# Performance work log

Hardware: AMD Instinct MI355X
Metric: run time of the kernel (lower is better)

The kernel has to match this reference:

```python
import jax, jax.numpy as jnp
import numpy as np

N = 16384      # number of target nodes
NS = 16384     # number of source nodes
K = 32         # neighbors per node
CS = 256       # source_channels
CT = 256       # target_channels
CO = 64        # out_channels
M = 64         # size (number of weight matrices); must equal CO for the original code to broadcast


def setup_inputs() -> dict:
    key = jax.random.key(0)
    ks = jax.random.split(key, 9)
    source = jax.random.normal(ks[0], (NS, CS), dtype=jnp.float32)
    target = jax.random.normal(ks[1], (N, CT), dtype=jnp.float32)
    neighbors = jax.random.randint(ks[2], (N, K), 0, NS)
    # size parallel Linear(CS, CO) layers, stored [in, out]
    W_lin = jax.random.normal(ks[3], (M, CS, CO), dtype=jnp.float32) / np.sqrt(CS)
    b_lin = jax.random.normal(ks[4], (M, CO), dtype=jnp.float32) * 0.01
    # source assignment Linear(CS, M)
    W_s = jax.random.normal(ks[5], (CS, M), dtype=jnp.float32) / np.sqrt(CS)
    b_s = jax.random.normal(ks[6], (M,), dtype=jnp.float32) * 0.01
    # target assignment Linear(CT, M)
    W_t = jax.random.normal(ks[7], (CT, M), dtype=jnp.float32) / np.sqrt(CT)
    b_t = jax.random.normal(ks[8], (M,), dtype=jnp.float32) * 0.01
    return {"source": source, "target": target, "neighbors": neighbors,
            "W_lin": W_lin, "b_lin": b_lin, "W_s": W_s, "b_s": b_s,
            "W_t": W_t, "b_t": b_t}


def reference(source, target, neighbors, W_lin, b_lin, W_s, b_s, W_t, b_t):
    # gather neighbor messages: [N, K, CS]
    msgs = source[neighbors]
    # assignment logits: source proj [N, K, M] + target proj broadcast [N, 1, M]
    s_logit = jnp.einsum('nkc,cm->nkm', msgs, W_s) + b_s
    t_logit = target @ W_t + b_t                      # [N, M]
    assignment = jax.nn.softmax(s_logit + t_logit[:, None, :], axis=-1)  # [N, K, M]
    # (assignment * stack_m(msgs @ W_m)).mean over m == assignment * (msgs @ mean_m W_m)
    # because assignment is independent of m (faithful to the original math).
    W_mean = W_lin.mean(axis=0)                       # [CS, CO]
    b_mean = b_lin.mean(axis=0)                       # [CO]
    proj = jnp.einsum('nkc,co->nko', msgs, W_mean) + b_mean  # [N, K, CO]
    return assignment * proj                          # [N, K, CO]  (CO == M)
```

## Files before the change

kernel.cpp:

```cpp
#include <hip/hip_runtime.h>
#include <hip/hip_fp16.h>

typedef _Float16 f16x8 __attribute__((ext_vector_type(8)));
typedef _Float16 f16x4 __attribute__((ext_vector_type(4)));
typedef float f32x4 __attribute__((ext_vector_type(4)));

__global__ void prep_weights(const float* __restrict__ W_lin, const float* __restrict__ b_lin,
                             const float* __restrict__ W_s, const float* __restrict__ W_t,
                             _Float16* __restrict__ WcT, _Float16* __restrict__ Wt16,
                             float* __restrict__ bmean) {
    int tid = blockIdx.x * 256 + threadIdx.x;
    if (tid < 16384) {
        int c = tid >> 6, o = tid & 63;
        WcT[o * 256 + c]  = (_Float16)W_s[c * 64 + o];
        Wt16[o * 256 + c] = (_Float16)W_t[c * 64 + o];
    } else {
        int t = tid - 16384;
        int c = t >> 6, o = t & 63;
        float s = 0.f;
        #pragma unroll 8
        for (int m = 0; m < 64; ++m) s += W_lin[m * 16384 + c * 64 + o];
        WcT[(64 + o) * 256 + c] = (_Float16)(s * (1.f / 64.f));
    }
    if (tid < 64) {
        float s = 0.f;
        #pragma unroll 8
        for (int m = 0; m < 64; ++m) s += b_lin[m * 64 + tid];
        bmean[tid] = s * (1.f / 64.f);
    }
}

__device__ __forceinline__ f16x8 cvt8(const float* p) {
    f32x4 x = *(const f32x4*)p;
    f32x4 y = *(const f32x4*)(p + 4);
    f16x8 h;
    h[0] = (_Float16)x[0]; h[1] = (_Float16)x[1]; h[2] = (_Float16)x[2]; h[3] = (_Float16)x[3];
    h[4] = (_Float16)y[0]; h[5] = (_Float16)y[1]; h[6] = (_Float16)y[2]; h[7] = (_Float16)y[3];
    return h;
}

__global__ __launch_bounds__(256, 2)
void gemm_prep(const float* __restrict__ source, const float* __restrict__ target,
               const _Float16* __restrict__ WcT, const _Float16* __restrict__ Wt16,
               const float* __restrict__ bmean, const float* __restrict__ b_s,
               const float* __restrict__ b_t,
               _Float16* __restrict__ Pe, _Float16* __restrict__ Pp,
               float* __restrict__ Et) {
    __shared__ _Float16 lds[32768];

    const int tid = threadIdx.x;
    const int w = tid >> 6, l = tid & 63;
    const int l15 = l & 15, lq = l >> 4;
    const int b = blockIdx.x;

    if (b < 256) {
        const int rb = b * 64;
        const float* arow = source + (size_t)(rb + w * 16 + l15) * 256;
        f16x8 af[8];
        #pragma unroll
        for (int s = 0; s < 8; ++s) af[s] = cvt8(arow + s * 32 + lq * 8);

        #pragma unroll
        for (int i = 0; i < 16; ++i) {
            int c = i * 256 + tid;
            int fi = c >> 6, lane = c & 63;
            int nt = fi >> 3, s = fi & 7;
            f16x8 v = *(const f16x8*)(WcT + (nt * 16 + (lane & 15)) * 256 + s * 32 + (lane >> 4) * 8);
            *(f16x8*)((char*)lds + c * 16) = v;
        }
        __syncthreads();

        const char* bb = (const char*)lds + l * 16;
        f32x4 acc[8] = {};
        #pragma unroll
        for (int s = 0; s < 8; ++s) {
            #pragma unroll
            for (int nt = 0; nt < 8; ++nt) {
                f16x8 bf = *(const f16x8*)(bb + nt * 8192 + s * 1024);
                acc[nt] = __builtin_amdgcn_mfma_f32_16x16x32_f16(af[s], bf, acc[nt], 0, 0, 0);
            }
        }

        float bmv[4];
        #pragma unroll
        for (int nt = 0; nt < 4; ++nt) bmv[nt] = bmean[nt * 16 + l15];
        #pragma unroll
        for (int j = 0; j < 4; ++j) {
            int row = rb + w * 16 + lq * 4 + j;
            #pragma unroll
            for (int nt = 0; nt < 4; ++nt) {
                Pe[row * 64 + nt * 16 + l15] = (_Float16)__expf(acc[nt][j]);
                Pp[row * 64 + nt * 16 + l15] = (_Float16)(acc[nt + 4][j] + bmv[nt]);
            }
        }
    } else {
        const int rb = (b - 256) * 64;
        const float* arow = target + (size_t)(rb + w * 16 + l15) * 256;
        f16x8 af[8];
        #pragma unroll
        for (int s = 0; s < 8; ++s) af[s] = cvt8(arow + s * 32 + lq * 8);

        #pragma unroll
        for (int i = 0; i < 8; ++i) {
            int c = i * 256 + tid;
            int fi = c >> 6, lane = c & 63;
            int nt = fi >> 3, s = fi & 7;
            f16x8 v = *(const f16x8*)(Wt16 + (nt * 16 + (lane & 15)) * 256 + s * 32 + (lane >> 4) * 8);
            *(f16x8*)((char*)lds + c * 16) = v;
        }
        __syncthreads();

        const char* bb = (const char*)lds + l * 16;
        f32x4 acc[4] = {};
        #pragma unroll
        for (int s = 0; s < 8; ++s) {
            #pragma unroll
            for (int nt = 0; nt < 4; ++nt) {
                f16x8 bf = *(const f16x8*)(bb + nt * 8192 + s * 1024);
                acc[nt] = __builtin_amdgcn_mfma_f32_16x16x32_f16(af[s], bf, acc[nt], 0, 0, 0);
            }
        }

        float bsv[4];
        #pragma unroll
        for (int nt = 0; nt < 4; ++nt) {
            int col = nt * 16 + l15;
            bsv[nt] = b_s[col] + b_t[col];
        }
        #pragma unroll
        for (int j = 0; j < 4; ++j) {
            int row = rb + w * 16 + lq * 4 + j;
            #pragma unroll
            for (int nt = 0; nt < 4; ++nt)
                Et[row * 64 + nt * 16 + l15] = __expf(acc[nt][j] + bsv[nt]);
        }
    }
}

__global__ __launch_bounds__(256)
void epilogue(const int* __restrict__ neighbors, const _Float16* __restrict__ Pe,
              const _Float16* __restrict__ Pp, const float* __restrict__ Et,
              float* __restrict__ out) {
    const int tid = threadIdx.x;
    const int w = tid >> 6, l = tid & 63;
    const int lq = l >> 4, l15 = l & 15;
    const int n = blockIdx.x * 4 + w;
    const int co = l15 * 4;

    f32x4 et = *(const f32x4*)(Et + n * 64 + co);

    int nb[8];
    #pragma unroll
    for (int g = 0; g < 8; ++g) nb[g] = neighbors[n * 32 + g * 4 + lq];

    f16x4 pe[8], pp[8];
    #pragma unroll
    for (int g = 0; g < 2; ++g) {
        pe[g] = *(const f16x4*)(Pe + nb[g] * 64 + co);
        pp[g] = *(const f16x4*)(Pp + nb[g] * 64 + co);
    }

    #pragma unroll
    for (int g = 0; g < 8; ++g) {
        if (g + 2 < 8) {
            pe[g + 2] = *(const f16x4*)(Pe + nb[g + 2] * 64 + co);
            pp[g + 2] = *(const f16x4*)(Pp + nb[g + 2] * 64 + co);
        }
        float w0 = (float)pe[g][0] * et[0];
        float w1 = (float)pe[g][1] * et[1];
        float w2 = (float)pe[g][2] * et[2];
        float w3 = (float)pe[g][3] * et[3];
        float s = (w0 + w1) + (w2 + w3);
        s += __shfl_xor(s, 1);
        s += __shfl_xor(s, 2);
        s += __shfl_xor(s, 4);
        s += __shfl_xor(s, 8);
        float inv = 1.0f / s;
        f32x4 o;
        o[0] = w0 * inv * (float)pp[g][0];
        o[1] = w1 * inv * (float)pp[g][1];
        o[2] = w2 * inv * (float)pp[g][2];
        o[3] = w3 * inv * (float)pp[g][3];
        *(f32x4*)(out + (size_t)(n * 32 + g * 4 + lq) * 64 + co) = o;
    }
}

extern "C" void kernel_launch(void* const* d_in, const int* in_sizes, int n_in,
                              void* d_out, int out_size, void* d_ws, size_t ws_size,
                              hipStream_t stream) {
    const float* source    = (const float*)d_in[0];
    const float* target    = (const float*)d_in[1];
    const int*   neighbors = (const int*)d_in[2];
    const float* W_lin     = (const float*)d_in[3];
    const float* b_lin     = (const float*)d_in[4];
    const float* W_s       = (const float*)d_in[5];
    const float* b_s       = (const float*)d_in[6];
    const float* W_t       = (const float*)d_in[7];
    const float* b_t       = (const float*)d_in[8];

    char* ws = (char*)d_ws;
    _Float16* Pe    = (_Float16*)ws;
    _Float16* Pp    = (_Float16*)(ws + (2u << 20));
    float*    Et    = (float*)(ws + (4u << 20));
    _Float16* WcT   = (_Float16*)(ws + (8u << 20));
    _Float16* Wt16  = (_Float16*)(ws + (8u << 20) + 65536);
    float*    bmean = (float*)(ws + (8u << 20) + 98304);
    float*    out   = (float*)d_out;

    prep_weights<<<128, 256, 0, stream>>>(W_lin, b_lin, W_s, W_t, WcT, Wt16, bmean);
    gemm_prep<<<512, 256, 0, stream>>>(source, target, WcT, Wt16, bmean, b_s, b_t,
                                       Pe, Pp, Et);
    epilogue<<<4096, 256, 0, stream>>>(neighbors, Pe, Pp, Et, out);
}
```

Before: 55.43 us.

## Interleave Pe/Pp rows, drop LDS staging, split GEMM columns across waves

```diff
diff --git a/kernel.cpp b/kernel.cpp
--- a/kernel.cpp
+++ b/kernel.cpp
@@ -39,108 +39,81 @@
     return h;
 }
 
-__global__ __launch_bounds__(256, 2)
+__global__ __launch_bounds__(256, 4)
 void gemm_prep(const float* __restrict__ source, const float* __restrict__ target,
                const _Float16* __restrict__ WcT, const _Float16* __restrict__ Wt16,
                const float* __restrict__ bmean, const float* __restrict__ b_s,
                const float* __restrict__ b_t,
-               _Float16* __restrict__ Pe, _Float16* __restrict__ Pp,
-               float* __restrict__ Et) {
-    __shared__ _Float16 lds[32768];
-
+               _Float16* __restrict__ Ppe, float* __restrict__ Et) {
     const int tid = threadIdx.x;
     const int w = tid >> 6, l = tid & 63;
     const int l15 = l & 15, lq = l >> 4;
     const int b = blockIdx.x;
 
-    if (b < 256) {
-        const int rb = b * 64;
-        const float* arow = source + (size_t)(rb + w * 16 + l15) * 256;
+    if (b < 1024) {
+        const int rb = b * 16;
+        const float* arow = source + (size_t)(rb + l15) * 256;
         f16x8 af[8];
         #pragma unroll
         for (int s = 0; s < 8; ++s) af[s] = cvt8(arow + s * 32 + lq * 8);
 
-        #pragma unroll
-        for (int i = 0; i < 16; ++i) {
-            int c = i * 256 + tid;
-            int fi = c >> 6, lane = c & 63;
-            int nt = fi >> 3, s = fi & 7;
-            f16x8 v = *(const f16x8*)(WcT + (nt * 16 + (lane & 15)) * 256 + s * 32 + (lane >> 4) * 8);
-            *(f16x8*)((char*)lds + c * 16) = v;
-        }
-        __syncthreads();
+        const int nt0 = w * 2;
+        const _Float16* b0p = WcT + (nt0 * 16 + l15) * 256 + lq * 8;
+        const _Float16* b1p = b0p + 16 * 256;
 
-        const char* bb = (const char*)lds + l * 16;
-        f32x4 acc[8] = {};
+        f32x4 acc[2] = {};
         #pragma unroll
         for (int s = 0; s < 8; ++s) {
-            #pragma unroll
-            for (int nt = 0; nt < 8; ++nt) {
-                f16x8 bf = *(const f16x8*)(bb + nt * 8192 + s * 1024);
-                acc[nt] = __builtin_amdgcn_mfma_f32_16x16x32_f16(af[s], bf, acc[nt], 0, 0, 0);
-            }
+            f16x8 b0 = *(const f16x8*)(b0p + s * 32);
+            f16x8 b1 = *(const f16x8*)(b1p + s * 32);
+            acc[0] = __builtin_amdgcn_mfma_f32_16x16x32_f16(af[s], b0, acc[0], 0, 0, 0);
+            acc[1] = __builtin_amdgcn_mfma_f32_16x16x32_f16(af[s], b1, acc[1], 0, 0, 0);
         }
 
-        float bmv[4];
+        const bool isPe = (nt0 < 4);
+        float addv[2];
         #pragma unroll
-        for (int nt = 0; nt < 4; ++nt) bmv[nt] = bmean[nt * 16 + l15];
+        for (int t = 0; t < 2; ++t)
+            addv[t] = isPe ? 0.f : bmean[(nt0 + t - 4) * 16 + l15];
+
         #pragma unroll
         for (int j = 0; j < 4; ++j) {
-            int row = rb + w * 16 + lq * 4 + j;
+            int row = rb + lq * 4 + j;
             #pragma unroll
-            for (int nt = 0; nt < 4; ++nt) {
-                Pe[row * 64 + nt * 16 + l15] = (_Float16)__expf(acc[nt][j]);
-                Pp[row * 64 + nt * 16 + l15] = (_Float16)(acc[nt + 4][j] + bmv[nt]);
+            for (int t = 0; t < 2; ++t) {
+                float v = acc[t][j];
+                _Float16 r = isPe ? (_Float16)__expf(v) : (_Float16)(v + addv[t]);
+                Ppe[row * 128 + (nt0 + t) * 16 + l15] = r;
             }
         }
     } else {
-        const int rb = (b - 256) * 64;
-        const float* arow = target + (size_t)(rb + w * 16 + l15) * 256;
+        const int rb = (b - 1024) * 16;
+        const float* arow = target + (size_t)(rb + l15) * 256;
         f16x8 af[8];
         #pragma unroll
         for (int s = 0; s < 8; ++s) af[s] = cvt8(arow + s * 32 + lq * 8);
 
-        #pragma unroll
-        for (int i = 0; i < 8; ++i) {
-            int c = i * 256 + tid;
-            int fi = c >> 6, lane = c & 63;
-            int nt = fi >> 3, s = fi & 7;
-            f16x8 v = *(const f16x8*)(Wt16 + (nt * 16 + (lane & 15)) * 256 + s * 32 + (lane >> 4) * 8);
-            *(f16x8*)((char*)lds + c * 16) = v;
-        }
-        __syncthreads();
-
-        const char* bb = (const char*)lds + l * 16;
-        f32x4 acc[4] = {};
+        const _Float16* bp = Wt16 + (w * 16 + l15) * 256 + lq * 8;
+        f32x4 acc = {};
         #pragma unroll
         for (int s = 0; s < 8; ++s) {
-            #pragma unroll
-            for (int nt = 0; nt < 4; ++nt) {
-                f16x8 bf = *(const f16x8*)(bb + nt * 8192 + s * 1024);
-                acc[nt] = __builtin_amdgcn_mfma_f32_16x16x32_f16(af[s], bf, acc[nt], 0, 0, 0);
-            }
+            f16x8 bf = *(const f16x8*)(bp + s * 32);
+            acc = __builtin_amdgcn_mfma_f32_16x16x32_f16(af[s], bf, acc, 0, 0, 0);
         }
 
-        float bsv[4];
-        #pragma unroll
-        for (int nt = 0; nt < 4; ++nt) {
-            int col = nt * 16 + l15;
-            bsv[nt] = b_s[col] + b_t[col];
-        }
+        const int col = w * 16 + l15;
+        const float bsv = b_s[col] + b_t[col];
         #pragma unroll
         for (int j = 0; j < 4; ++j) {
-            int row = rb + w * 16 + lq * 4 + j;
-            #pragma unroll
-            for (int nt = 0; nt < 4; ++nt)
-                Et[row * 64 + nt * 16 + l15] = __expf(acc[nt][j] + bsv[nt]);
+            int row = rb + lq * 4 + j;
+            Et[row * 64 + col] = __expf(acc[j] + bsv);
         }
     }
 }
 
 __global__ __launch_bounds__(256)
-void epilogue(const int* __restrict__ neighbors, const _Float16* __restrict__ Pe,
-              const _Float16* __restrict__ Pp, const float* __restrict__ Et,
-              float* __restrict__ out) {
+void epilogue(const int* __restrict__ neighbors, const _Float16* __restrict__ Ppe,
+              const float* __restrict__ Et, float* __restrict__ out) {
     const int tid = threadIdx.x;
     const int w = tid >> 6, l = tid & 63;
     const int lq = l >> 4, l15 = l & 15;
@@ -156,15 +129,15 @@
     f16x4 pe[8], pp[8];
     #pragma unroll
     for (int g = 0; g < 2; ++g) {
-        pe[g] = *(const f16x4*)(Pe + nb[g] * 64 + co);
-        pp[g] = *(const f16x4*)(Pp + nb[g] * 64 + co);
+        pe[g] = *(const f16x4*)(Ppe + nb[g] * 128 + co);
+        pp[g] = *(const f16x4*)(Ppe + nb[g] * 128 + 64 + co);
     }
 
     #pragma unroll
     for (int g = 0; g < 8; ++g) {
         if (g + 2 < 8) {
-            pe[g + 2] = *(const f16x4*)(Pe + nb[g + 2] * 64 + co);
-            pp[g + 2] = *(const f16x4*)(Pp + nb[g + 2] * 64 + co);
+            pe[g + 2] = *(const f16x4*)(Ppe + nb[g + 2] * 128 + co);
+            pp[g + 2] = *(const f16x4*)(Ppe + nb[g + 2] * 128 + 64 + co);
         }
         float w0 = (float)pe[g][0] * et[0];
         float w1 = (float)pe[g][1] * et[1];
@@ -181,7 +154,7 @@
         o[1] = w1 * inv * (float)pp[g][1];
         o[2] = w2 * inv * (float)pp[g][2];
         o[3] = w3 * inv * (float)pp[g][3];
-        *(f32x4*)(out + (size_t)(n * 32 + g * 4 + lq) * 64 + co) = o;
+        __builtin_nontemporal_store(o, (f32x4*)(out + (size_t)(n * 32 + g * 4 + lq) * 64 + co));
     }
 }
 
@@ -199,8 +172,7 @@
     const float* b_t       = (const float*)d_in[8];
 
     char* ws = (char*)d_ws;
-    _Float16* Pe    = (_Float16*)ws;
-    _Float16* Pp    = (_Float16*)(ws + (2u << 20));
+    _Float16* Ppe   = (_Float16*)ws;
     float*    Et    = (float*)(ws + (4u << 20));
     _Float16* WcT   = (_Float16*)(ws + (8u << 20));
     _Float16* Wt16  = (_Float16*)(ws + (8u << 20) + 65536);
@@ -208,7 +180,7 @@
     float*    out   = (float*)d_out;
 
     prep_weights<<<128, 256, 0, stream>>>(W_lin, b_lin, W_s, W_t, WcT, Wt16, bmean);
-    gemm_prep<<<512, 256, 0, stream>>>(source, target, WcT, Wt16, bmean, b_s, b_t,
-                                       Pe, Pp, Et);
-    epilogue<<<4096, 256, 0, stream>>>(neighbors, Pe, Pp, Et, out);
+    gemm_prep<<<2048, 256, 0, stream>>>(source, target, WcT, Wt16, bmean, b_s, b_t,
+                                        Ppe, Et);
+    epilogue<<<4096, 256, 0, stream>>>(neighbors, Ppe, Et, out);
 }
```

New measurement: 64.78 us. 16.9% more time.

## Interleave Pe/Pp rows and process two nodes per wave with all gathers issued upfront

Applied to the files above, without the earlier changes.

```diff
diff --git a/kernel.cpp b/kernel.cpp
--- a/kernel.cpp
+++ b/kernel.cpp
@@ -44,8 +44,7 @@
                const _Float16* __restrict__ WcT, const _Float16* __restrict__ Wt16,
                const float* __restrict__ bmean, const float* __restrict__ b_s,
                const float* __restrict__ b_t,
-               _Float16* __restrict__ Pe, _Float16* __restrict__ Pp,
-               float* __restrict__ Et) {
+               _Float16* __restrict__ Ppe, float* __restrict__ Et) {
     __shared__ _Float16 lds[32768];
 
     const int tid = threadIdx.x;
@@ -89,8 +88,8 @@
             int row = rb + w * 16 + lq * 4 + j;
             #pragma unroll
             for (int nt = 0; nt < 4; ++nt) {
-                Pe[row * 64 + nt * 16 + l15] = (_Float16)__expf(acc[nt][j]);
-                Pp[row * 64 + nt * 16 + l15] = (_Float16)(acc[nt + 4][j] + bmv[nt]);
+                Ppe[row * 128 + nt * 16 + l15]        = (_Float16)__expf(acc[nt][j]);
+                Ppe[row * 128 + (nt + 4) * 16 + l15]  = (_Float16)(acc[nt + 4][j] + bmv[nt]);
             }
         }
     } else {
@@ -138,38 +137,41 @@
 }
 
 __global__ __launch_bounds__(256)
-void epilogue(const int* __restrict__ neighbors, const _Float16* __restrict__ Pe,
-              const _Float16* __restrict__ Pp, const float* __restrict__ Et,
-              float* __restrict__ out) {
+void epilogue(const int* __restrict__ neighbors, const _Float16* __restrict__ Ppe,
+              const float* __restrict__ Et, float* __restrict__ out) {
     const int tid = threadIdx.x;
     const int w = tid >> 6, l = tid & 63;
     const int lq = l >> 4, l15 = l & 15;
-    const int n = blockIdx.x * 4 + w;
+    const int n0 = blockIdx.x * 8 + w * 2;
     const int co = l15 * 4;
 
-    f32x4 et = *(const f32x4*)(Et + n * 64 + co);
-
-    int nb[8];
-    #pragma unroll
-    for (int g = 0; g < 8; ++g) nb[g] = neighbors[n * 32 + g * 4 + lq];
-
-    f16x4 pe[8], pp[8];
-    #pragma unroll
-    for (int g = 0; g < 2; ++g) {
-        pe[g] = *(const f16x4*)(Pe + nb[g] * 64 + co);
-        pp[g] = *(const f16x4*)(Pp + nb[g] * 64 + co);
-    }
-
-    #pragma unroll
-    for (int g = 0; g < 8; ++g) {
-        if (g + 2 < 8) {
-            pe[g + 2] = *(const f16x4*)(Pe + nb[g + 2] * 64 + co);
-            pp[g + 2] = *(const f16x4*)(Pp + nb[g + 2] * 64 + co);
-        }
-        float w0 = (float)pe[g][0] * et[0];
-        float w1 = (float)pe[g][1] * et[1];
-        float w2 = (float)pe[g][2] * et[2];
-        float w3 = (float)pe[g][3] * et[3];
+    f32x4 et0 = *(const f32x4*)(Et + n0 * 64 + co);
+    f32x4 et1 = *(const f32x4*)(Et + (n0 + 1) * 64 + co);
+
+    int nb0[8], nb1[8];
+    #pragma unroll
+    for (int g = 0; g < 8; ++g) nb0[g] = neighbors[n0 * 32 + g * 4 + lq];
+    #pragma unroll
+    for (int g = 0; g < 8; ++g) nb1[g] = neighbors[(n0 + 1) * 32 + g * 4 + lq];
+
+    f16x4 pe0[8], pp0[8], pe1[8], pp1[8];
+    #pragma unroll
+    for (int g = 0; g < 8; ++g) {
+        pe0[g] = *(const f16x4*)(Ppe + nb0[g] * 128 + co);
+        pp0[g] = *(const f16x4*)(Ppe + nb0[g] * 128 + 64 + co);
+    }
+    #pragma unroll
+    for (int g = 0; g < 8; ++g) {
+        pe1[g] = *(const f16x4*)(Ppe + nb1[g] * 128 + co);
+        pp1[g] = *(const f16x4*)(Ppe + nb1[g] * 128 + 64 + co);
+    }
+
+    #pragma unroll
+    for (int g = 0; g < 8; ++g) {
+        float w0 = (float)pe0[g][0] * et0[0];
+        float w1 = (float)pe0[g][1] * et0[1];
+        float w2 = (float)pe0[g][2] * et0[2];
+        float w3 = (float)pe0[g][3] * et0[3];
         float s = (w0 + w1) + (w2 + w3);
         s += __shfl_xor(s, 1);
         s += __shfl_xor(s, 2);
@@ -177,11 +179,30 @@
         s += __shfl_xor(s, 8);
         float inv = 1.0f / s;
         f32x4 o;
-        o[0] = w0 * inv * (float)pp[g][0];
-        o[1] = w1 * inv * (float)pp[g][1];
-        o[2] = w2 * inv * (float)pp[g][2];
-        o[3] = w3 * inv * (float)pp[g][3];
-        *(f32x4*)(out + (size_t)(n * 32 + g * 4 + lq) * 64 + co) = o;
+        o[0] = w0 * inv * (float)pp0[g][0];
+        o[1] = w1 * inv * (float)pp0[g][1];
+        o[2] = w2 * inv * (float)pp0[g][2];
+        o[3] = w3 * inv * (float)pp0[g][3];
+        *(f32x4*)(out + (size_t)(n0 * 32 + g * 4 + lq) * 64 + co) = o;
+    }
+    #pragma unroll
+    for (int g = 0; g < 8; ++g) {
+        float w0 = (float)pe1[g][0] * et1[0];
+        float w1 = (float)pe1[g][1] * et1[1];
+        float w2 = (float)pe1[g][2] * et1[2];
+        float w3 = (float)pe1[g][3] * et1[3];
+        float s = (w0 + w1) + (w2 + w3);
+        s += __shfl_xor(s, 1);
+        s += __shfl_xor(s, 2);
+        s += __shfl_xor(s, 4);
+        s += __shfl_xor(s, 8);
+        float inv = 1.0f / s;
+        f32x4 o;
+        o[0] = w0 * inv * (float)pp1[g][0];
+        o[1] = w1 * inv * (float)pp1[g][1];
+        o[2] = w2 * inv * (float)pp1[g][2];
+        o[3] = w3 * inv * (float)pp1[g][3];
+        *(f32x4*)(out + (size_t)((n0 + 1) * 32 + g * 4 + lq) * 64 + co) = o;
     }
 }
 
@@ -199,8 +220,7 @@
     const float* b_t       = (const float*)d_in[8];
 
     char* ws = (char*)d_ws;
-    _Float16* Pe    = (_Float16*)ws;
-    _Float16* Pp    = (_Float16*)(ws + (2u << 20));
+    _Float16* Ppe   = (_Float16*)ws;
     float*    Et    = (float*)(ws + (4u << 20));
     _Float16* WcT   = (_Float16*)(ws + (8u << 20));
     _Float16* Wt16  = (_Float16*)(ws + (8u << 20) + 65536);
@@ -209,6 +229,6 @@
 
     prep_weights<<<128, 256, 0, stream>>>(W_lin, b_lin, W_s, W_t, WcT, Wt16, bmean);
     gemm_prep<<<512, 256, 0, stream>>>(source, target, WcT, Wt16, bmean, b_s, b_t,
-                                       Pe, Pp, Et);
-    epilogue<<<4096, 256, 0, stream>>>(neighbors, Pe, Pp, Et, out);
-}
+                                       Ppe, Et);
+    epilogue<<<2048, 256, 0, stream>>>(neighbors, Ppe, Et, out);
+}
```

New measurement: 54.13 us. 2.4% less time.
